# Optimization experiments

Measured on AMD Instinct MI355X. Metric: run time of the kernel, lower is better.

## Reference

```python
import jax, jax.numpy as jnp
import numpy as np

N = 50000
E = 800000
D_IN = 64
D_OUT = 64


def setup_inputs() -> dict:
    key = jax.random.key(0)
    k_x, k_e, k_ws, k_bs, k_wn, k_bn = jax.random.split(key, 6)
    x = jax.random.normal(k_x, (N, D_IN), dtype=jnp.float32)
    edge_index = jax.random.randint(k_e, (2, E), 0, N, dtype=jnp.int64)
    # nn.Linear params: weight [out, in], bias [out]
    lim = 1.0 / np.sqrt(D_IN)
    W_self = jax.random.uniform(k_ws, (D_OUT, D_IN), minval=-lim, maxval=lim, dtype=jnp.float32)
    b_self = jax.random.uniform(k_bs, (D_OUT,), minval=-lim, maxval=lim, dtype=jnp.float32)
    W_neigh = jax.random.uniform(k_wn, (D_OUT, D_IN), minval=-lim, maxval=lim, dtype=jnp.float32)
    b_neigh = jax.random.uniform(k_bn, (D_OUT,), minval=-lim, maxval=lim, dtype=jnp.float32)
    return {"x": x, "edge_index": edge_index, "W_self": W_self, "b_self": b_self,
            "W_neigh": W_neigh, "b_neigh": b_neigh}


def reference(x, edge_index, W_self, b_self, W_neigh, b_neigh):
    row, col = edge_index[0], edge_index[1]
    n = x.shape[0]
    # degree of each destination node (clamped to 1)
    deg = jax.ops.segment_sum(jnp.ones_like(row, dtype=x.dtype), row, num_segments=n)
    deg = jnp.maximum(deg, 1.0)
    # mean-aggregate neighbor features: scatter-add x[col] into row buckets
    agg = jax.ops.segment_sum(x[col], row, num_segments=n)  # [N, D_IN]
    agg = agg / deg[:, None]
    out = x @ W_self.T + b_self + agg @ W_neigh.T + b_neigh
    return out
```

## Files before the change

### kernel.cpp

```cpp
#include <hip/hip_runtime.h>
#include <hip/hip_bf16.h>


#define D    64
#define CAP  64
#define TPW  16
#define BKN  64
#define SLP  66
#define EPT  8
#define CAPB 4608

typedef __attribute__((ext_vector_type(8))) short bf16x8;
typedef __attribute__((ext_vector_type(4))) float f32x4;

__device__ __forceinline__ unsigned short f2bf(float f) {
    unsigned u = __float_as_uint(f);
    return (unsigned short)((u + 0x7fffu + ((u >> 16) & 1u)) >> 16);
}
__device__ __forceinline__ float bf2f(unsigned short s) {
    return __uint_as_float((unsigned)s << 16);
}
__device__ __forceinline__ int load_idx(const void* ei, int use64, long long pos) {
    if (use64) return (int)((const long long*)ei)[pos];
    return ((const int*)ei)[pos];
}

__global__ __launch_bounds__(256) void bin_k(
        const float* __restrict__ x, const void* __restrict__ ei,
        unsigned* __restrict__ staging, unsigned* __restrict__ gcur,
        unsigned short* __restrict__ xb, int N, int E, int NBr) {
    __shared__ unsigned lcnt[256];
    __shared__ unsigned lbase[256];
    __shared__ int s_use64;
    const int t = threadIdx.x;
    lcnt[t] = 0u;
    if (t < 64) {
        long long v = (t < 16) ? ((const long long*)ei)[t] : 0;
        unsigned long long bad = __ballot(t < 16 && (v < 0 || v >= (long long)N));
        if (t == 0) s_use64 = (bad == 0ULL) ? 1 : 0;
    }
    __syncthreads();
    const int use64 = s_use64;
    const int e0 = blockIdx.x * (256 * EPT);
    unsigned pk[EPT], lp[EPT];
    int bk[EPT];
    #pragma unroll
    for (int j = 0; j < EPT; ++j) {
        int e = e0 + j * 256 + t;
        if (e < E) {
            int r = load_idx(ei, use64, e);
            int c = load_idx(ei, use64, (long long)E + e);
            pk[j] = ((unsigned)r << 16) | (unsigned)(c & 0xffff);
            bk[j] = r >> 8;
            lp[j] = atomicAdd(&lcnt[bk[j]], 1u);
        } else bk[j] = -1;
    }
    __syncthreads();
    if (t < NBr) {
        unsigned n = lcnt[t];
        lbase[t] = n ? atomicAdd(&gcur[t], n) : 0u;
    }
    __syncthreads();
    #pragma unroll
    for (int j = 0; j < EPT; ++j) {
        if (bk[j] >= 0) {
            unsigned p = lbase[bk[j]] + lp[j];
            if (p < CAPB) staging[(unsigned)bk[j] * CAPB + p] = pk[j];
        }
    }
    int tid = blockIdx.x * 256 + t;
    int NT  = gridDim.x * 256;
    int NV  = (N * D) >> 2;
    for (int i = tid; i < NV; i += NT) {
        float4 v = *(const float4*)&x[i * 4];
        ushort4 o;
        o.x = f2bf(v.x); o.y = f2bf(v.y); o.z = f2bf(v.z); o.w = f2bf(v.w);
        *(ushort4*)&xb[i * 4] = o;
    }
}

__global__ __launch_bounds__(256) void fuse2_k(
        const unsigned short* __restrict__ xb,
        const unsigned* __restrict__ staging, const unsigned* __restrict__ gcur,
        const float* __restrict__ Ws, const float* __restrict__ bs,
        const float* __restrict__ Wn, const float* __restrict__ bn,
        float* __restrict__ out, int N) {
    __shared__ __align__(16) short wcat[D][136];
    __shared__ __align__(16) short mtile[2][TPW][72];
    __shared__ unsigned short sl[BKN * SLP];
    __shared__ unsigned scnt[BKN];

    const int t = threadIdx.x;
    for (int i = t; i < D * 128; i += 256) {
        int f = i >> 7, kk = i & 127;
        float v = (kk < D) ? Ws[f * D + kk] : Wn[f * D + (kk - D)];
        wcat[f][kk] = (short)f2bf(v);
    }
    if (t < BKN) scnt[t] = 0u;
    __syncthreads();

    const int node0 = blockIdx.x * BKN;
    const int q = blockIdx.x >> 2;
    unsigned nstg = gcur[q]; if (nstg > CAPB) nstg = CAPB;
    const unsigned* sbase = staging + (size_t)q * CAPB;
    for (unsigned e = t; e < nstg; e += 256) {
        unsigned pk = sbase[e];
        int local = (int)(pk >> 16) - node0;
        if ((unsigned)local < (unsigned)BKN) {
            unsigned pos = atomicAdd(&scnt[local], 1u);
            if (pos < CAP) sl[local * SLP + pos] = (unsigned short)(pk & 0xffffu);
        }
    }
    __syncthreads();

    const int w    = t >> 6;
    const int lane = t & 63;
    const int m_   = lane & 15;
    const int quad = lane >> 4;
    const int ql   = m_;
    const int q4   = quad;
    const int pair = w >> 1;
    const int half = w & 1;

    for (int it = 0; it < 2; ++it) {
        const int tile = node0 + (it * 2 + pair) * TPW;

        #pragma unroll
        for (int pp = 0; pp < 2; ++pp) {
            int p = half * 2 + pp;
            int n = tile + p * 4 + q4;
            int nl = n - node0;
            int deg = (n < N) ? (int)scnt[nl] : 0;
            int mm = deg < CAP ? deg : CAP;
            float4 s = make_float4(0.f, 0.f, 0.f, 0.f);
            for (int seg = 0; seg < mm; seg += 16) {
                int sv = (seg + ql < mm) ? (int)sl[nl * SLP + seg + ql] : 0;
                int mq = mm - seg; if (mq > 16) mq = 16;
                unsigned off[16];
                #pragma unroll
                for (int j = 0; j < 16; ++j) {
                    int c = __shfl(sv, (q4 << 4) + j);
                    off[j] = (unsigned)c * D + 4 * ql;
                }
                ushort4 v[16];
                #pragma unroll
                for (int j = 0; j < 16; ++j)
                    v[j] = *(const ushort4*)&xb[off[j]];
                #pragma unroll
                for (int j = 0; j < 16; ++j) {
                    float m = (j < mq) ? 1.0f : 0.0f;
                    s.x = fmaf(m, bf2f(v[j].x), s.x);
                    s.y = fmaf(m, bf2f(v[j].y), s.y);
                    s.z = fmaf(m, bf2f(v[j].z), s.z);
                    s.w = fmaf(m, bf2f(v[j].w), s.w);
                }
            }
            float dinv = (deg > 0) ? 1.0f / (float)deg : 0.0f;
            short4 mv;
            mv.x = (short)f2bf(s.x * dinv); mv.y = (short)f2bf(s.y * dinv);
            mv.z = (short)f2bf(s.z * dinv); mv.w = (short)f2bf(s.w * dinv);
            *(short4*)&mtile[pair][p * 4 + q4][4 * ql] = mv;
        }
        __syncthreads();

        int nrow = tile + m_;
        const unsigned short* xr = xb + (size_t)(nrow < N ? nrow : 0) * D;
        bf16x8 afrag[4];
        afrag[0] = *(const bf16x8*)&xr[quad * 8];
        afrag[1] = *(const bf16x8*)&xr[32 + quad * 8];
        #pragma unroll
        for (int ks = 2; ks < 4; ++ks)
            afrag[ks] = *(const bf16x8*)&mtile[pair][m_][(ks - 2) * 32 + quad * 8];

        f32x4 acc[2];
        #pragma unroll
        for (int i = 0; i < 2; ++i) {
            int fcol = (half * 2 + i) * 16 + m_;
            float bsum = bs[fcol] + bn[fcol];
            acc[i] = (f32x4){bsum, bsum, bsum, bsum};
        }
        #pragma unroll
        for (int i = 0; i < 2; ++i) {
            int nf = half * 2 + i;
            #pragma unroll
            for (int ks = 0; ks < 4; ++ks) {
                bf16x8 bfr = *(const bf16x8*)&wcat[nf * 16 + m_][ks * 32 + quad * 8];
                acc[i] = __builtin_amdgcn_mfma_f32_16x16x32_bf16(
                    afrag[ks], bfr, acc[i], 0, 0, 0);
            }
        }

        #pragma unroll
        for (int i = 0; i < 2; ++i) {
            int fcol = (half * 2 + i) * 16 + m_;
            #pragma unroll
            for (int r = 0; r < 4; ++r) {
                int node = tile + quad * 4 + r;
                if (node < N) out[(size_t)node * D + fcol] = acc[i][r];
            }
        }
        __syncthreads();
    }
}

extern "C" void kernel_launch(void* const* d_in, const int* in_sizes, int n_in,
                              void* d_out, int out_size, void* d_ws, size_t ws_size,
                              hipStream_t stream) {
    const float* x  = (const float*)d_in[0];
    const void*  ei = d_in[1];
    const float* Ws = (const float*)d_in[2];
    const float* bs = (const float*)d_in[3];
    const float* Wn = (const float*)d_in[4];
    const float* bn = (const float*)d_in[5];
    float* out = (float*)d_out;

    int N = in_sizes[0] / D;
    int E = in_sizes[1] / 2;

    int NBr = (N + 255) >> 8;
    unsigned short* xb      = (unsigned short*)d_ws;
    unsigned*       staging = (unsigned*)(xb + (size_t)N * D);
    unsigned*       gcur    = staging + (size_t)NBr * CAPB;

    hipMemsetAsync(gcur, 0, (size_t)NBr * sizeof(unsigned), stream);

    int binb = (E + 256 * EPT - 1) / (256 * EPT);
    bin_k<<<binb, 256, 0, stream>>>(x, ei, staging, gcur, xb, N, E, NBr);

    int fblocks = (N + BKN - 1) / BKN;
    fuse2_k<<<fblocks, 256, 0, stream>>>(xb, staging, gcur,
                                         Ws, bs, Wn, bn, out, N);
}
```

Measured before the change: 133.2 us.

## Fuse binning and aggregation kernels into one kernel with a grid-wide barrier

Merges the edge-binning/bf16-conversion kernel and the aggregate-plus-MFMA kernel into a single kernel. Blocks first take conversion slices and edge chunks from a shared work list, then wait on a global done counter used as a grid barrier before the aggregation phase. It also remaps block indices across XCDs for locality and unrolls the staging reads four-wide. The goal is to remove the launch gap and tail between the two kernels and to reuse the weight tile load. The cost is a spin barrier that only works if every block is resident at once, plus an LDS union.

```diff
diff --git a/kernel.cpp b/kernel.cpp
--- a/kernel.cpp
+++ b/kernel.cpp
@@ -8,7 +8,9 @@
 #define BKN  64
 #define SLP  66
 #define EPT  8
+#define CHUNK (256 * EPT)
 #define CAPB 4608
+#define CSLICE 16384
 
 typedef __attribute__((ext_vector_type(8))) short bf16x8;
 typedef __attribute__((ext_vector_type(4))) float f32x4;
@@ -25,90 +27,129 @@
     return ((const int*)ei)[pos];
 }
 
-__global__ __launch_bounds__(256) void bin_k(
+__global__ __launch_bounds__(256, 4) void mega_k(
         const float* __restrict__ x, const void* __restrict__ ei,
         unsigned* __restrict__ staging, unsigned* __restrict__ gcur,
-        unsigned short* __restrict__ xb, int N, int E, int NBr) {
-    __shared__ unsigned lcnt[256];
-    __shared__ unsigned lbase[256];
+        unsigned* __restrict__ done, unsigned short* __restrict__ xb,
+        const float* __restrict__ Ws, const float* __restrict__ bs,
+        const float* __restrict__ Wn, const float* __restrict__ bn,
+        float* __restrict__ out, int N, int E, int NBr,
+        int NV, int NCI, int nitems) {
+    __shared__ __align__(16) short wcat[D][136];
+    __shared__ __align__(16) short mtile[2][TPW][72];
+    __shared__ union {
+        struct { unsigned lcnt[256]; unsigned lbase[256]; } bin;
+        struct { unsigned scnt[BKN]; unsigned short sl[BKN * SLP]; } bkt;
+    } u;
     __shared__ int s_use64;
     const int t = threadIdx.x;
-    lcnt[t] = 0u;
+
     if (t < 64) {
         long long v = (t < 16) ? ((const long long*)ei)[t] : 0;
         unsigned long long bad = __ballot(t < 16 && (v < 0 || v >= (long long)N));
         if (t == 0) s_use64 = (bad == 0ULL) ? 1 : 0;
     }
-    __syncthreads();
-    const int use64 = s_use64;
-    const int e0 = blockIdx.x * (256 * EPT);
-    unsigned pk[EPT], lp[EPT];
-    int bk[EPT];
-    #pragma unroll
-    for (int j = 0; j < EPT; ++j) {
-        int e = e0 + j * 256 + t;
-        if (e < E) {
-            int r = load_idx(ei, use64, e);
-            int c = load_idx(ei, use64, (long long)E + e);
-            pk[j] = ((unsigned)r << 16) | (unsigned)(c & 0xffff);
-            bk[j] = r >> 8;
-            lp[j] = atomicAdd(&lcnt[bk[j]], 1u);
-        } else bk[j] = -1;
-    }
-    __syncthreads();
-    if (t < NBr) {
-        unsigned n = lcnt[t];
-        lbase[t] = n ? atomicAdd(&gcur[t], n) : 0u;
-    }
-    __syncthreads();
-    #pragma unroll
-    for (int j = 0; j < EPT; ++j) {
-        if (bk[j] >= 0) {
-            unsigned p = lbase[bk[j]] + lp[j];
-            if (p < CAPB) staging[(unsigned)bk[j] * CAPB + p] = pk[j];
-        }
-    }
-    int tid = blockIdx.x * 256 + t;
-    int NT  = gridDim.x * 256;
-    int NV  = (N * D) >> 2;
-    for (int i = tid; i < NV; i += NT) {
-        float4 v = *(const float4*)&x[i * 4];
-        ushort4 o;
-        o.x = f2bf(v.x); o.y = f2bf(v.y); o.z = f2bf(v.z); o.w = f2bf(v.w);
-        *(ushort4*)&xb[i * 4] = o;
-    }
-}
-
-__global__ __launch_bounds__(256) void fuse2_k(
-        const unsigned short* __restrict__ xb,
-        const unsigned* __restrict__ staging, const unsigned* __restrict__ gcur,
-        const float* __restrict__ Ws, const float* __restrict__ bs,
-        const float* __restrict__ Wn, const float* __restrict__ bn,
-        float* __restrict__ out, int N) {
-    __shared__ __align__(16) short wcat[D][136];
-    __shared__ __align__(16) short mtile[2][TPW][72];
-    __shared__ unsigned short sl[BKN * SLP];
-    __shared__ unsigned scnt[BKN];
-
-    const int t = threadIdx.x;
     for (int i = t; i < D * 128; i += 256) {
         int f = i >> 7, kk = i & 127;
         float v = (kk < D) ? Ws[f * D + kk] : Wn[f * D + (kk - D)];
         wcat[f][kk] = (short)f2bf(v);
     }
-    if (t < BKN) scnt[t] = 0u;
-    __syncthreads();
-
-    const int node0 = blockIdx.x * BKN;
-    const int q = blockIdx.x >> 2;
-    unsigned nstg = gcur[q]; if (nstg > CAPB) nstg = CAPB;
-    const unsigned* sbase = staging + (size_t)q * CAPB;
-    for (unsigned e = t; e < nstg; e += 256) {
-        unsigned pk = sbase[e];
-        int local = (int)(pk >> 16) - node0;
-        if ((unsigned)local < (unsigned)BKN) {
-            unsigned pos = atomicAdd(&scnt[local], 1u);
-            if (pos < CAP) sl[local * SLP + pos] = (unsigned short)(pk & 0xffffu);
+    __syncthreads();
+    const int use64 = s_use64;
+
+    for (int it = blockIdx.x; it < nitems; it += gridDim.x) {
+        if (it < NCI) {
+            int i0 = it * CSLICE;
+            int i1 = i0 + CSLICE; if (i1 > NV) i1 = NV;
+            for (int i = i0 + t; i < i1; i += 256) {
+                float4 v = *(const float4*)&x[i * 4];
+                ushort4 o;
+                o.x = f2bf(v.x); o.y = f2bf(v.y);
+                o.z = f2bf(v.z); o.w = f2bf(v.w);
+                *(ushort4*)&xb[i * 4] = o;
+            }
+        } else {
+            int ch = it - NCI;
+            u.bin.lcnt[t] = 0u;
+            __syncthreads();
+            const int e0 = ch * CHUNK;
+            unsigned pk[EPT], lp[EPT];
+            int bk[EPT];
+            #pragma unroll
+            for (int j = 0; j < EPT; ++j) {
+                int e = e0 + j * 256 + t;
+                if (e < E) {
+                    int r = load_idx(ei, use64, e);
+                    int c = load_idx(ei, use64, (long long)E + e);
+                    pk[j] = ((unsigned)r << 16) | (unsigned)(c & 0xffff);
+                    bk[j] = r >> 8;
+                    lp[j] = atomicAdd(&u.bin.lcnt[bk[j]], 1u);
+                } else bk[j] = -1;
+            }
+            __syncthreads();
+            if (t < NBr) {
+                unsigned n = u.bin.lcnt[t];
+                u.bin.lbase[t] = n ? atomicAdd(&gcur[t], n) : 0u;
+            }
+            __syncthreads();
+            #pragma unroll
+            for (int j = 0; j < EPT; ++j) {
+                if (bk[j] >= 0) {
+                    unsigned p = u.bin.lbase[bk[j]] + lp[j];
+                    if (p < CAPB) staging[(unsigned)bk[j] * CAPB + p] = pk[j];
+                }
+            }
+        }
+        __syncthreads();
+        if (t == 0) {
+            __threadfence();
+            __hip_atomic_fetch_add(done, 1u, __ATOMIC_RELAXED,
+                                   __HIP_MEMORY_SCOPE_AGENT);
+        }
+    }
+
+    if (t == 0) {
+        while (__hip_atomic_load(done, __ATOMIC_RELAXED,
+                                 __HIP_MEMORY_SCOPE_AGENT) < (unsigned)nitems)
+            __builtin_amdgcn_s_sleep(2);
+        (void)__hip_atomic_load(done, __ATOMIC_ACQUIRE,
+                                __HIP_MEMORY_SCOPE_AGENT);
+    }
+    __syncthreads();
+
+    const int nb  = gridDim.x;
+    const int q8  = nb >> 3, r8 = nb & 7;
+    const int xcd = blockIdx.x & 7, idx = blockIdx.x >> 3;
+    const int logical = (xcd < r8) ? xcd * (q8 + 1) + idx
+                                   : r8 * (q8 + 1) + (xcd - r8) * q8 + idx;
+    const int node0 = logical * BKN;
+    const int qb    = logical >> 2;
+
+    if (t < BKN) u.bkt.scnt[t] = 0u;
+    __syncthreads();
+    unsigned nstg = __hip_atomic_load(&gcur[qb], __ATOMIC_RELAXED,
+                                      __HIP_MEMORY_SCOPE_AGENT);
+    if (nstg > CAPB) nstg = CAPB;
+    const unsigned* sbase = staging + (size_t)qb * CAPB;
+    for (unsigned e = t; e < nstg; e += 1024u) {
+        unsigned pks[4]; int have[4];
+        #pragma unroll
+        for (int k = 0; k < 4; ++k) {
+            unsigned ee = e + (unsigned)k * 256u;
+            have[k] = (ee < nstg);
+            pks[k] = have[k] ? sbase[ee] : 0u;
+        }
+        #pragma unroll
+        for (int k = 0; k < 4; ++k) {
+            if (have[k]) {
+                int local = (int)(pks[k] >> 16) - node0;
+                if ((unsigned)local < (unsigned)BKN) {
+                    unsigned pos = atomicAdd(&u.bkt.scnt[local], 1u);
+                    if (pos < CAP)
+                        u.bkt.sl[local * SLP + pos] =
+                            (unsigned short)(pks[k] & 0xffffu);
+                }
+            }
         }
     }
     __syncthreads();
@@ -122,19 +163,19 @@
     const int pair = w >> 1;
     const int half = w & 1;
 
-    for (int it = 0; it < 2; ++it) {
-        const int tile = node0 + (it * 2 + pair) * TPW;
+    for (int itr = 0; itr < 2; ++itr) {
+        const int tile = node0 + (itr * 2 + pair) * TPW;
 
         #pragma unroll
         for (int pp = 0; pp < 2; ++pp) {
             int p = half * 2 + pp;
             int n = tile + p * 4 + q4;
             int nl = n - node0;
-            int deg = (n < N) ? (int)scnt[nl] : 0;
+            int deg = (n < N) ? (int)u.bkt.scnt[nl] : 0;
             int mm = deg < CAP ? deg : CAP;
             float4 s = make_float4(0.f, 0.f, 0.f, 0.f);
             for (int seg = 0; seg < mm; seg += 16) {
-                int sv = (seg + ql < mm) ? (int)sl[nl * SLP + seg + ql] : 0;
+                int sv = (seg + ql < mm) ? (int)u.bkt.sl[nl * SLP + seg + ql] : 0;
                 int mq = mm - seg; if (mq > 16) mq = 16;
                 unsigned off[16];
                 #pragma unroll
@@ -221,13 +262,17 @@
     unsigned short* xb      = (unsigned short*)d_ws;
     unsigned*       staging = (unsigned*)(xb + (size_t)N * D);
     unsigned*       gcur    = staging + (size_t)NBr * CAPB;
-
-    hipMemsetAsync(gcur, 0, (size_t)NBr * sizeof(unsigned), stream);
-
-    int binb = (E + 256 * EPT - 1) / (256 * EPT);
-    bin_k<<<binb, 256, 0, stream>>>(x, ei, staging, gcur, xb, N, E, NBr);
-
+    unsigned*       done    = gcur + NBr;
+
+    hipMemsetAsync(gcur, 0, (size_t)(NBr + 1) * sizeof(unsigned), stream);
+
+    int NV  = (N * D) >> 2;
+    int NCI = (NV + CSLICE - 1) / CSLICE;
+    int nch = (E + CHUNK - 1) / CHUNK;
+    int nitems  = NCI + nch;
     int fblocks = (N + BKN - 1) / BKN;
-    fuse2_k<<<fblocks, 256, 0, stream>>>(xb, staging, gcur,
-                                         Ws, bs, Wn, bn, out, N);
-}
+
+    mega_k<<<fblocks, 256, 0, stream>>>(x, ei, staging, gcur, done, xb,
+                                        Ws, bs, Wn, bn, out,
+                                        N, E, NBr, NV, NCI, nitems);
+}
```

Result: slower. 211.2 us (+58.6%).
